# Optimization experiments

Measured on AMD Instinct MI355X. Metric: run time of the kernel, lower is better.

## Reference

```python
import jax, jax.numpy as jnp
import numpy as np

ALPHA = 0.2  # LeakyReLU negative slope
MASK_VAL = -9e15


def setup_inputs() -> dict:
    key = jax.random.key(0)
    k1, k2, k3 = jax.random.split(key, 3)
    bs, N, d = 16, 1024, 128
    h = jax.random.normal(k1, (bs, N, d), dtype=jnp.float32)
    # nn.Linear(in, out, bias=False).weight has shape [out, in]
    W = jax.random.normal(k2, (d, d), dtype=jnp.float32) * (1.414 / np.sqrt(d))
    # a: Linear(2*out, 1) -> weight [1, 2d] flattened to [2d], bias [1]
    a_w = jax.random.normal(k3, (2 * d,), dtype=jnp.float32) * 0.1
    a_b = jnp.zeros((1,), dtype=jnp.float32)
    return {"h": h, "W": W, "a_w": a_w, "a_b": a_b}


def reference(h, W, a_w, a_b):
    # h: [bs, N, d], W: [d, d] (torch Linear weight), a_w: [2d], a_b: [1]
    bs, N, d = h.shape
    Wh = jnp.einsum('bnd,fd->bnf', h, W)  # [bs, N, d]
    # Decompose a([Wh_i ; Wh_j]) = Wh_i . a1 + Wh_j . a2 + b  (avoids O(N^2 * 2d) concat)
    a1, a2 = a_w[:d], a_w[d:]
    s1 = Wh @ a1  # [bs, N] -- source-node contribution (row index i)
    s2 = Wh @ a2  # [bs, N] -- target-node contribution (col index j)
    e = jax.nn.leaky_relu(s1[:, :, None] + s2[:, None, :] + a_b[0], negative_slope=ALPHA)
    # adj = ones - eye: mask out the diagonal (self-edges)
    diag = jnp.eye(N, dtype=bool)
    e = jnp.where(diag[None, :, :], MASK_VAL, e)
    attention = jax.nn.softmax(e, axis=-1)  # [bs, N, N]
    h_prime = jnp.einsum('bij,bjf->bif', attention, Wh)
    return jax.nn.elu(h_prime)  # concat=True applies ELU
```

## Files before the change

### kernel.cpp

```cpp
#include <hip/hip_runtime.h>
#include <hip/hip_bf16.h>
#include <stdint.h>

#define LOG2E 1.4426950408889634f

typedef float f32x4 __attribute__((ext_vector_type(4)));
typedef short s16x8 __attribute__((ext_vector_type(8)));

__device__ __forceinline__ float bf2f(uint16_t u) {
    uint32_t x = ((uint32_t)u) << 16;
    float f;
    __builtin_memcpy(&f, &x, 4);
    return f;
}
__device__ __forceinline__ uint16_t f2bf(float f) {
    uint32_t x;
    __builtin_memcpy(&x, &f, 4);
    uint32_t r = (x + 0x7fffu + ((x >> 16) & 1u)) >> 16;
    return (uint16_t)r;
}

__global__ __launch_bounds__(256) void k0_splitW(
    const float* __restrict__ W, uint16_t* __restrict__ whi, uint16_t* __restrict__ wlo)
{
    int i = blockIdx.x * 256 + threadIdx.x;
    float x = W[i];
    uint16_t hb = f2bf(x);
    whi[i] = hb;
    wlo[i] = f2bf(x - bf2f(hb));
}

__global__ __launch_bounds__(256) void k1_gemm(
    const float* __restrict__ h, const uint16_t* __restrict__ whi_,
    const uint16_t* __restrict__ wlo_,
    const float* __restrict__ aw, const float* __restrict__ ab,
    uint16_t* __restrict__ whB, float* __restrict__ s1b, float* __restrict__ s2g)
{
    __shared__ float sred[2][2][16][2];
    const int tid = threadIdx.x;
    const int w = tid >> 6, lane = tid & 63;
    const int q = lane >> 4, n16 = lane & 15;
    const int rg = w >> 1, fh = w & 1;
    const int R0 = blockIdx.x * 32 + rg * 16;
    const int f0 = fh * 64;

    f32x4 acc[4];
#pragma unroll
    for (int i = 0; i < 4; ++i) acc[i] = 0.f;

    const float* hrow = h + (size_t)(R0 + n16) * 128 + q * 8;
    const uint16_t* whbase = whi_ + (size_t)(f0 + n16) * 128 + q * 8;
    const uint16_t* wlbase = wlo_ + (size_t)(f0 + n16) * 128 + q * 8;
#pragma unroll
    for (int kc = 0; kc < 4; ++kc) {
        float4 x0 = *(const float4*)(hrow + kc * 32);
        float4 x1 = *(const float4*)(hrow + kc * 32 + 4);
        float xs[8] = {x0.x, x0.y, x0.z, x0.w, x1.x, x1.y, x1.z, x1.w};
        s16x8 ahi, alo;
#pragma unroll
        for (int t = 0; t < 8; ++t) {
            uint16_t hb = f2bf(xs[t]);
            ahi[t] = (short)hb;
            alo[t] = (short)f2bf(xs[t] - bf2f(hb));
        }
#pragma unroll
        for (int fb = 0; fb < 4; ++fb) {
            s16x8 bhi = *(const s16x8*)(whbase + fb * 16 * 128 + kc * 32);
            s16x8 blo = *(const s16x8*)(wlbase + fb * 16 * 128 + kc * 32);
            acc[fb] = __builtin_amdgcn_mfma_f32_16x16x32_bf16(ahi, bhi, acc[fb], 0, 0, 0);
            acc[fb] = __builtin_amdgcn_mfma_f32_16x16x32_bf16(alo, bhi, acc[fb], 0, 0, 0);
            acc[fb] = __builtin_amdgcn_mfma_f32_16x16x32_bf16(ahi, blo, acc[fb], 0, 0, 0);
        }
    }

    float s1p[4] = {0.f, 0.f, 0.f, 0.f}, s2p[4] = {0.f, 0.f, 0.f, 0.f};
#pragma unroll
    for (int fb = 0; fb < 4; ++fb) {
        float a1 = aw[f0 + fb * 16 + n16];
        float a2 = aw[128 + f0 + fb * 16 + n16];
#pragma unroll
        for (int reg = 0; reg < 4; ++reg) {
            s1p[reg] = fmaf(acc[fb][reg], a1, s1p[reg]);
            s2p[reg] = fmaf(acc[fb][reg], a2, s2p[reg]);
        }
    }
#pragma unroll
    for (int off = 1; off < 16; off <<= 1) {
#pragma unroll
        for (int reg = 0; reg < 4; ++reg) {
            s1p[reg] += __shfl_xor(s1p[reg], off);
            s2p[reg] += __shfl_xor(s2p[reg], off);
        }
    }
    if (n16 == 0) {
#pragma unroll
        for (int reg = 0; reg < 4; ++reg) {
            sred[rg][fh][q * 4 + reg][0] = s1p[reg];
            sred[rg][fh][q * 4 + reg][1] = s2p[reg];
        }
    }
    __syncthreads();
    if (tid < 32) {
        int rg2 = tid >> 4, il = tid & 15;
        float s1 = sred[rg2][0][il][0] + sred[rg2][1][il][0];
        float s2 = sred[rg2][0][il][1] + sred[rg2][1][il][1];
        int R = blockIdx.x * 32 + rg2 * 16 + il;
        s1b[R] = LOG2E * (s1 + ab[0]);
        s2g[R] = LOG2E * s2;
    }

    const int b = R0 >> 10;
    const int jt = (R0 & 1023) >> 5;
    uint16_t* base = whB + (size_t)b * 131072 + (size_t)jt * 512;
    const int lane8p = (rg * 2 + (q >> 1)) * 16 + n16;
#pragma unroll
    for (int fb = 0; fb < 4; ++fb) {
        int fblk = fh * 4 + fb;
        uint32_t e0 = f2bf(acc[fb][0]), e1 = f2bf(acc[fb][1]);
        uint32_t e2 = f2bf(acc[fb][2]), e3 = f2bf(acc[fb][3]);
        uint2 val = make_uint2(e0 | (e1 << 16), e2 | (e3 << 16));
        *(uint2*)(base + fblk * 16384 + lane8p * 8 + (q & 1) * 4) = val;
    }
}

__global__ __launch_bounds__(256) void k1b_top2(
    const float* __restrict__ s2g, float* __restrict__ smax1,
    float* __restrict__ smax2, int* __restrict__ imax)
{
    __shared__ float sv1[4], sv2[4];
    __shared__ int si1[4];
    const int b = blockIdx.x, t = threadIdx.x;
    const float* s2 = s2g + b * 1024;
    float v1 = -3e38f, v2 = -3e38f;
    int i1 = 0;
    float4 vv = *(const float4*)(s2 + t * 4);
    float vs[4] = {vv.x, vv.y, vv.z, vv.w};
#pragma unroll
    for (int r = 0; r < 4; ++r) {
        float v = vs[r];
        if (v > v1) { v2 = v1; v1 = v; i1 = t * 4 + r; }
        else if (v > v2) v2 = v;
    }
#pragma unroll
    for (int off = 1; off < 64; off <<= 1) {
        float w1 = __shfl_xor(v1, off);
        float w2 = __shfl_xor(v2, off);
        int wi = __shfl_xor(i1, off);
        if (w1 > v1) { v2 = fmaxf(v1, w2); v1 = w1; i1 = wi; }
        else { v2 = fmaxf(v2, w1); }
    }
    if ((t & 63) == 0) { sv1[t >> 6] = v1; sv2[t >> 6] = v2; si1[t >> 6] = i1; }
    __syncthreads();
    if (t == 0) {
        float b1 = sv1[0], b2 = sv2[0];
        int bi = si1[0];
#pragma unroll
        for (int k = 1; k < 4; ++k) {
            float w1 = sv1[k], w2 = sv2[k];
            int wi = si1[k];
            if (w1 > b1) { b2 = fmaxf(b1, w2); b1 = w1; bi = wi; }
            else { b2 = fmaxf(b2, w1); }
        }
        smax1[b] = b1; smax2[b] = b2; imax[b] = bi;
    }
}

__global__ __launch_bounds__(64) void k2_attn(
    const uint16_t* __restrict__ whB, const float* __restrict__ s1b,
    const float* __restrict__ s2g, const float* __restrict__ smax1,
    const float* __restrict__ smax2, const int* __restrict__ imax,
    float* __restrict__ out)
{
    const int lane = threadIdx.x;
    const int q = lane >> 4, n16 = lane & 15;
    const int idx = blockIdx.x;
    const int rowbase = (idx >> 1) * 16;
    const int fh = idx & 1;
    const int b = rowbase >> 10, jb = b * 1024;

    const int iRow = rowbase + n16;
    const int ji = iRow & 1023;
    const float s1v = s1b[iRow];
    const float Mi = (imax[b] == ji) ? smax2[b] : smax1[b];
    const float tm = s1v + Mi;
    const float mi = fmaxf(tm, 0.2f * tm);
    const float Ai = s1v - mi;
    const float Bi = fmaf(0.2f, s1v, -mi);
    float l = 0.f;
    f32x4 acc[4];
#pragma unroll
    for (int i = 0; i < 4; ++i) acc[i] = 0.f;

    const uint16_t* wb = whB + (size_t)b * 131072 + (size_t)lane * 8;
    const float* ug = s2g + jb + q * 8;

    for (int jt = 0; jt < 32; ++jt) {
        const int J0 = jt * 32;
        float4 ua = *(const float4*)(ug + J0);
        float4 ub = *(const float4*)(ug + J0 + 4);
        float uv[8] = {ua.x, ua.y, ua.z, ua.w, ub.x, ub.y, ub.z, ub.w};
        s16x8 A;
#pragma unroll
        for (int t = 0; t < 8; ++t) {
            float arg = fmaxf(Ai + uv[t], fmaf(0.2f, uv[t], Bi));
            float p = __builtin_amdgcn_exp2f(arg);
            if (J0 + q * 8 + t == ji) p = 0.f;
            uint16_t pb = f2bf(p);
            l += bf2f(pb);
            A[t] = (short)pb;
        }
        const uint16_t* bp = wb + (size_t)jt * 512;
#pragma unroll
        for (int fb = 0; fb < 4; ++fb) {
            s16x8 B = *(const s16x8*)(bp + (size_t)(fh * 4 + fb) * 16384);
            acc[fb] = __builtin_amdgcn_mfma_f32_16x16x32_bf16(A, B, acc[fb], 0, 0, 0);
        }
    }

    l += __shfl_xor(l, 16);
    l += __shfl_xor(l, 32);
    float rl[4];
#pragma unroll
    for (int reg = 0; reg < 4; ++reg)
        rl[reg] = 1.0f / __shfl(l, q * 4 + reg);

    const int f0 = fh * 64;
#pragma unroll
    for (int fb = 0; fb < 4; ++fb) {
#pragma unroll
        for (int reg = 0; reg < 4; ++reg) {
            float v = acc[fb][reg] * rl[reg];
            float e = v > 0.f ? v : (__builtin_amdgcn_exp2f(v * LOG2E) - 1.f);
            int row = rowbase + q * 4 + reg;
            out[(size_t)row * 128 + f0 + fb * 16 + n16] = e;
        }
    }
}

extern "C" void kernel_launch(void* const* d_in, const int* in_sizes, int n_in,
                              void* d_out, int out_size, void* d_ws, size_t ws_size,
                              hipStream_t stream) {
    (void)in_sizes; (void)n_in; (void)out_size; (void)ws_size;
    const float* h  = (const float*)d_in[0];
    const float* W  = (const float*)d_in[1];
    const float* aw = (const float*)d_in[2];
    const float* ab = (const float*)d_in[3];
    float* out = (float*)d_out;

    uint16_t* whB = (uint16_t*)d_ws;
    float* s1b   = (float*)((char*)d_ws + (4u << 20));
    float* s2g   = s1b + 16384;
    float* smax1 = s2g + 16384;
    float* smax2 = smax1 + 16;
    int*   imax  = (int*)(smax2 + 16);
    uint16_t* whi = (uint16_t*)(imax + 16);
    uint16_t* wlo = whi + 16384;

    k0_splitW<<<64, 256, 0, stream>>>(W, whi, wlo);
    k1_gemm<<<512, 256, 0, stream>>>(h, whi, wlo, aw, ab, whB, s1b, s2g);
    k1b_top2<<<16, 256, 0, stream>>>(s2g, smax1, smax2, imax);
    k2_attn<<<2048, 64, 0, stream>>>(whB, s1b, s2g, smax1, smax2, imax, out);
}
```

Baseline: 100.1 us.

## Fuse column-max into GEMM, drop top2 kernel, split features finer with XCD-aware mapping

```diff
diff --git a/kernel.cpp b/kernel.cpp
--- a/kernel.cpp
+++ b/kernel.cpp
@@ -34,19 +34,18 @@
     const float* __restrict__ h, const uint16_t* __restrict__ whi_,
     const uint16_t* __restrict__ wlo_,
     const float* __restrict__ aw, const float* __restrict__ ab,
-    uint16_t* __restrict__ whB, float* __restrict__ s1b, float* __restrict__ s2g)
+    uint16_t* __restrict__ whB, float* __restrict__ s1b, float* __restrict__ s2g,
+    float* __restrict__ smaxrg)
 {
-    __shared__ float sred[2][2][16][2];
+    __shared__ float sred[4][16][2];
     const int tid = threadIdx.x;
     const int w = tid >> 6, lane = tid & 63;
     const int q = lane >> 4, n16 = lane & 15;
-    const int rg = w >> 1, fh = w & 1;
-    const int R0 = blockIdx.x * 32 + rg * 16;
-    const int f0 = fh * 64;
-
-    f32x4 acc[4];
-#pragma unroll
-    for (int i = 0; i < 4; ++i) acc[i] = 0.f;
+    const int R0 = blockIdx.x * 16;
+    const int f0 = w * 32;
+
+    f32x4 acc[2];
+    acc[0] = 0.f; acc[1] = 0.f;
 
     const float* hrow = h + (size_t)(R0 + n16) * 128 + q * 8;
     const uint16_t* whbase = whi_ + (size_t)(f0 + n16) * 128 + q * 8;
@@ -64,7 +63,7 @@
             alo[t] = (short)f2bf(xs[t] - bf2f(hb));
         }
 #pragma unroll
-        for (int fb = 0; fb < 4; ++fb) {
+        for (int fb = 0; fb < 2; ++fb) {
             s16x8 bhi = *(const s16x8*)(whbase + fb * 16 * 128 + kc * 32);
             s16x8 blo = *(const s16x8*)(wlbase + fb * 16 * 128 + kc * 32);
             acc[fb] = __builtin_amdgcn_mfma_f32_16x16x32_bf16(ahi, bhi, acc[fb], 0, 0, 0);
@@ -75,7 +74,7 @@
 
     float s1p[4] = {0.f, 0.f, 0.f, 0.f}, s2p[4] = {0.f, 0.f, 0.f, 0.f};
 #pragma unroll
-    for (int fb = 0; fb < 4; ++fb) {
+    for (int fb = 0; fb < 2; ++fb) {
         float a1 = aw[f0 + fb * 16 + n16];
         float a2 = aw[128 + f0 + fb * 16 + n16];
 #pragma unroll
@@ -95,27 +94,33 @@
     if (n16 == 0) {
 #pragma unroll
         for (int reg = 0; reg < 4; ++reg) {
-            sred[rg][fh][q * 4 + reg][0] = s1p[reg];
-            sred[rg][fh][q * 4 + reg][1] = s2p[reg];
+            sred[w][q * 4 + reg][0] = s1p[reg];
+            sred[w][q * 4 + reg][1] = s2p[reg];
         }
     }
     __syncthreads();
-    if (tid < 32) {
-        int rg2 = tid >> 4, il = tid & 15;
-        float s1 = sred[rg2][0][il][0] + sred[rg2][1][il][0];
-        float s2 = sred[rg2][0][il][1] + sred[rg2][1][il][1];
-        int R = blockIdx.x * 32 + rg2 * 16 + il;
+    if (tid < 16) {
+        float s1 = sred[0][tid][0] + sred[1][tid][0] + sred[2][tid][0] + sred[3][tid][0];
+        float s2 = sred[0][tid][1] + sred[1][tid][1] + sred[2][tid][1] + sred[3][tid][1];
+        int R = R0 + tid;
         s1b[R] = LOG2E * (s1 + ab[0]);
-        s2g[R] = LOG2E * s2;
+        float s2s = LOG2E * s2;
+        s2g[R] = s2s;
+        float m = s2s;
+#pragma unroll
+        for (int off = 1; off < 16; off <<= 1)
+            m = fmaxf(m, __shfl_xor(m, off));
+        if (tid == 0) smaxrg[blockIdx.x] = m;
     }
 
     const int b = R0 >> 10;
     const int jt = (R0 & 1023) >> 5;
+    const int rg1 = (R0 >> 4) & 1;
     uint16_t* base = whB + (size_t)b * 131072 + (size_t)jt * 512;
-    const int lane8p = (rg * 2 + (q >> 1)) * 16 + n16;
-#pragma unroll
-    for (int fb = 0; fb < 4; ++fb) {
-        int fblk = fh * 4 + fb;
+    const int lane8p = (rg1 * 2 + (q >> 1)) * 16 + n16;
+#pragma unroll
+    for (int fb = 0; fb < 2; ++fb) {
+        int fblk = w * 2 + fb;
         uint32_t e0 = f2bf(acc[fb][0]), e1 = f2bf(acc[fb][1]);
         uint32_t e2 = f2bf(acc[fb][2]), e3 = f2bf(acc[fb][3]);
         uint2 val = make_uint2(e0 | (e1 << 16), e2 | (e3 << 16));
@@ -123,73 +128,36 @@
     }
 }
 
-__global__ __launch_bounds__(256) void k1b_top2(
-    const float* __restrict__ s2g, float* __restrict__ smax1,
-    float* __restrict__ smax2, int* __restrict__ imax)
-{
-    __shared__ float sv1[4], sv2[4];
-    __shared__ int si1[4];
-    const int b = blockIdx.x, t = threadIdx.x;
-    const float* s2 = s2g + b * 1024;
-    float v1 = -3e38f, v2 = -3e38f;
-    int i1 = 0;
-    float4 vv = *(const float4*)(s2 + t * 4);
-    float vs[4] = {vv.x, vv.y, vv.z, vv.w};
-#pragma unroll
-    for (int r = 0; r < 4; ++r) {
-        float v = vs[r];
-        if (v > v1) { v2 = v1; v1 = v; i1 = t * 4 + r; }
-        else if (v > v2) v2 = v;
-    }
-#pragma unroll
-    for (int off = 1; off < 64; off <<= 1) {
-        float w1 = __shfl_xor(v1, off);
-        float w2 = __shfl_xor(v2, off);
-        int wi = __shfl_xor(i1, off);
-        if (w1 > v1) { v2 = fmaxf(v1, w2); v1 = w1; i1 = wi; }
-        else { v2 = fmaxf(v2, w1); }
-    }
-    if ((t & 63) == 0) { sv1[t >> 6] = v1; sv2[t >> 6] = v2; si1[t >> 6] = i1; }
-    __syncthreads();
-    if (t == 0) {
-        float b1 = sv1[0], b2 = sv2[0];
-        int bi = si1[0];
-#pragma unroll
-        for (int k = 1; k < 4; ++k) {
-            float w1 = sv1[k], w2 = sv2[k];
-            int wi = si1[k];
-            if (w1 > b1) { b2 = fmaxf(b1, w2); b1 = w1; bi = wi; }
-            else { b2 = fmaxf(b2, w1); }
-        }
-        smax1[b] = b1; smax2[b] = b2; imax[b] = bi;
-    }
-}
-
 __global__ __launch_bounds__(64) void k2_attn(
     const uint16_t* __restrict__ whB, const float* __restrict__ s1b,
-    const float* __restrict__ s2g, const float* __restrict__ smax1,
-    const float* __restrict__ smax2, const int* __restrict__ imax,
+    const float* __restrict__ s2g, const float* __restrict__ smaxrg,
     float* __restrict__ out)
 {
     const int lane = threadIdx.x;
     const int q = lane >> 4, n16 = lane & 15;
     const int idx = blockIdx.x;
-    const int rowbase = (idx >> 1) * 16;
-    const int fh = idx & 1;
-    const int b = rowbase >> 10, jb = b * 1024;
+    const int xcd = idx & 7, o = idx >> 3;
+    const int b = xcd * 2 + (o >> 8);
+    const int rem = o & 255;
+    const int fq = rem >> 6, rg = rem & 63;
+    const int rowbase = b * 1024 + rg * 16;
+    const int jb = b * 1024;
+
+    float M = smaxrg[b * 64 + lane];
+#pragma unroll
+    for (int off = 1; off < 64; off <<= 1)
+        M = fmaxf(M, __shfl_xor(M, off));
 
     const int iRow = rowbase + n16;
     const int ji = iRow & 1023;
     const float s1v = s1b[iRow];
-    const float Mi = (imax[b] == ji) ? smax2[b] : smax1[b];
-    const float tm = s1v + Mi;
+    const float tm = s1v + M;
     const float mi = fmaxf(tm, 0.2f * tm);
     const float Ai = s1v - mi;
     const float Bi = fmaf(0.2f, s1v, -mi);
     float l = 0.f;
-    f32x4 acc[4];
-#pragma unroll
-    for (int i = 0; i < 4; ++i) acc[i] = 0.f;
+    f32x4 acc[2];
+    acc[0] = 0.f; acc[1] = 0.f;
 
     const uint16_t* wb = whB + (size_t)b * 131072 + (size_t)lane * 8;
     const float* ug = s2g + jb + q * 8;
@@ -211,8 +179,8 @@
         }
         const uint16_t* bp = wb + (size_t)jt * 512;
 #pragma unroll
-        for (int fb = 0; fb < 4; ++fb) {
-            s16x8 B = *(const s16x8*)(bp + (size_t)(fh * 4 + fb) * 16384);
+        for (int fb = 0; fb < 2; ++fb) {
+            s16x8 B = *(const s16x8*)(bp + (size_t)(fq * 2 + fb) * 16384);
             acc[fb] = __builtin_amdgcn_mfma_f32_16x16x32_bf16(A, B, acc[fb], 0, 0, 0);
         }
     }
@@ -224,9 +192,9 @@
     for (int reg = 0; reg < 4; ++reg)
         rl[reg] = 1.0f / __shfl(l, q * 4 + reg);
 
-    const int f0 = fh * 64;
-#pragma unroll
-    for (int fb = 0; fb < 4; ++fb) {
+    const int f0 = fq * 32;
+#pragma unroll
+    for (int fb = 0; fb < 2; ++fb) {
 #pragma unroll
         for (int reg = 0; reg < 4; ++reg) {
             float v = acc[fb][reg] * rl[reg];
@@ -248,16 +216,13 @@
     float* out = (float*)d_out;
 
     uint16_t* whB = (uint16_t*)d_ws;
-    float* s1b   = (float*)((char*)d_ws + (4u << 20));
-    float* s2g   = s1b + 16384;
-    float* smax1 = s2g + 16384;
-    float* smax2 = smax1 + 16;
-    int*   imax  = (int*)(smax2 + 16);
-    uint16_t* whi = (uint16_t*)(imax + 16);
+    float* s1b    = (float*)((char*)d_ws + (4u << 20));
+    float* s2g    = s1b + 16384;
+    float* smaxrg = s2g + 16384;
+    uint16_t* whi = (uint16_t*)(smaxrg + 1024);
     uint16_t* wlo = whi + 16384;
 
     k0_splitW<<<64, 256, 0, stream>>>(W, whi, wlo);
-    k1_gemm<<<512, 256, 0, stream>>>(h, whi, wlo, aw, ab, whB, s1b, s2g);
-    k1b_top2<<<16, 256, 0, stream>>>(s2g, smax1, smax2, imax);
-    k2_attn<<<2048, 64, 0, stream>>>(whB, s1b, s2g, smax1, smax2, imax, out);
-}
+    k1_gemm<<<1024, 256, 0, stream>>>(h, whi, wlo, aw, ab, whB, s1b, s2g, smaxrg);
+    k2_attn<<<4096, 64, 0, stream>>>(whB, s1b, s2g, smaxrg, out);
+}
```

Result: slower. 106.4 us (+6.3%).
